# Performance work log

Measured on AMD Instinct MI355X. Metric: run time of the kernel, lower is better.

The kernel has to match this reference:

```python
import jax, jax.numpy as jnp
import numpy as np

D_MODEL = 1024
LAYER_IDX = 5
D_FF = 4096
SPARSITY = 0.9
TOKENS = 8192
IN_UP = D_MODEL * (LAYER_IDX + 1)  # 6144


def _sparse_weight(rng, out_f, in_f, sparsity):
    """Row-wise k-sparse weight matrix mimicking SparseLinear's padded-CSR:
    each output row keeps k = round(in_f*(1-sparsity)) live columns,
    values ~ U(-b, b) with b = 1/sqrt(effective_fan_in)."""
    k = max(1, round(in_f * (1.0 - sparsity)))
    bound = 1.0 / np.sqrt(max(1.0, in_f * (1.0 - sparsity)))
    scores = rng.random((out_f, in_f))
    # top-k per row -> boolean mask
    thresh = np.partition(scores, in_f - k, axis=1)[:, in_f - k][:, None]
    mask = scores >= thresh
    W = (rng.uniform(-bound, bound, (out_f, in_f)).astype(np.float32)) * mask
    return jnp.asarray(W), jnp.asarray(mask)


def setup_inputs() -> dict:
    key = jax.random.key(0)
    x = jax.random.normal(key, (TOKENS, IN_UP), dtype=jnp.float32)
    rng = np.random.default_rng(0)
    W_up, mask_up = _sparse_weight(rng, D_FF, IN_UP, SPARSITY)
    W_down, mask_down = _sparse_weight(rng, D_MODEL, D_FF, SPARSITY)
    return {"ffn_input_cat": x, "W_up": W_up, "W_down": W_down,
            "mask_up": mask_up, "mask_down": mask_down}


def reference(ffn_input_cat, W_up, W_down, mask_up, mask_down):
    # fc_down(gelu(fc_up(x))); SparseLinear == masked dense linear, no bias.
    # torch F.gelu default is the exact (erf) gelu.
    h = jax.nn.gelu(ffn_input_cat @ (W_up * mask_up).T, approximate=False)  # [T, d_ff]
    return h @ (W_down * mask_down).T  # [T, d_model]
```

## Files before the change

kernel.cpp:

```cpp
#include <hip/hip_runtime.h>
#include <cstdint>
#include <cstddef>

typedef unsigned short u16;
typedef __attribute__((ext_vector_type(8))) short  bf16x8;
typedef __attribute__((ext_vector_type(4))) float  f32x4;
typedef __attribute__((ext_vector_type(4))) unsigned short u16x4;

__device__ __forceinline__ u16 f2bf(float f) {
    unsigned u = __float_as_uint(f);
    unsigned r = (u + 0x7FFFu + ((u >> 16) & 1u)) >> 16;
    return (u16)r;
}

__device__ __forceinline__ void async_lds16(const u16* g, u16* l) {
    __builtin_amdgcn_global_load_lds(
        (const __attribute__((address_space(1))) unsigned int*)g,
        (__attribute__((address_space(3))) unsigned int*)l,
        16, 0, 0);
}

__global__ __launch_bounds__(256) void cvt3_kernel(const float* __restrict__ s0, u16* __restrict__ d0, int n0,
                                                   const float* __restrict__ s1, u16* __restrict__ d1, int n1,
                                                   const float* __restrict__ s2, u16* __restrict__ d2, int n2) {
    const int total = n0 + n1 + n2;
    for (int i = blockIdx.x * 256 + threadIdx.x; i < total; i += gridDim.x * 256) {
        const float* s; u16* d; int j = i;
        if (j < n0)            { s = s0; d = d0; }
        else if (j < n0 + n1)  { s = s1; d = d1; j -= n0; }
        else                   { s = s2; d = d2; j -= n0 + n1; }
        float4 a = ((const float4*)s)[j];
        u16x4 o;
        o[0] = f2bf(a.x); o[1] = f2bf(a.y); o[2] = f2bf(a.z); o[3] = f2bf(a.w);
        ((u16x4*)d)[j] = o;
    }
}


template<bool GELU, typename OutT, int BN>
__global__ __launch_bounds__(512, 2) void gemm_q(const u16* __restrict__ A,
                                                 const u16* __restrict__ B,
                                                 OutT* __restrict__ C,
                                                 int K, int lda, int ldb, int ldc) {
    constexpr int NI  = BN / 64;
    constexpr int NQN = NI / 2;
    __shared__ __align__(16) u16 sA[2][256 * 64];
    __shared__ __align__(16) u16 sB[2][BN * 64];

    const int tid  = threadIdx.x;
    const int wave = tid >> 6;
    const int lane = tid & 63;
    const int quad = lane >> 4;
    const int r16  = lane & 15;

    const int nwg = gridDim.x * gridDim.y;
    int lin = blockIdx.y * gridDim.x + blockIdx.x;
    lin = (lin & 7) * (nwg >> 3) + (lin >> 3);
    const int n0 = (lin % gridDim.x) * BN;
    const int m0 = (lin / gridDim.x) * 256;

    const int wm = (wave >> 2) * 128;
    const int wn = (wave & 3) * (BN / 4);

    const int srow = tid >> 3;
    const int scol = (((tid & 7) ^ (srow & 7)) << 3);
    const u16* gAs = A + (size_t)(m0 + srow) * lda + scol;
    const u16* gBs = B + (size_t)(n0 + srow) * ldb + scol;

#define STAGE_A(dst, kt) { const size_t ko_ = (size_t)(kt) * 64; \
    _Pragma("unroll") for (int i_ = 0; i_ < 4; i_++) \
        async_lds16(gAs + (size_t)(i_ * 64) * lda + ko_, (dst) + i_ * 4096 + tid * 8); }
#define STAGE_B(dst, kt) { const size_t ko_ = (size_t)(kt) * 64; \
    _Pragma("unroll") for (int i_ = 0; i_ < NI; i_++) \
        async_lds16(gBs + (size_t)(i_ * 64) * ldb + ko_, (dst) + i_ * 4096 + tid * 8); }

    const int g0 = (quad ^ (r16 & 7)) << 3;
    const int g1 = g0 ^ 32;

    struct FragT { bf16x8 a[4][2]; bf16x8 b[NQN][2]; };

#define READQ(F, Ab, Bb, qmi, qni) { \
    _Pragma("unroll") for (int i_ = 0; i_ < 4; i_++) { \
        const int ao_ = (wm + ((qmi) * 4 + i_) * 16 + r16) * 64; \
        F.a[i_][0] = *(const bf16x8*)&(Ab)[ao_ + g0]; \
        F.a[i_][1] = *(const bf16x8*)&(Ab)[ao_ + g1]; } \
    _Pragma("unroll") for (int i_ = 0; i_ < NQN; i_++) { \
        const int bo_ = (wn + ((qni) * NQN + i_) * 16 + r16) * 64; \
        F.b[i_][0] = *(const bf16x8*)&(Bb)[bo_ + g0]; \
        F.b[i_][1] = *(const bf16x8*)&(Bb)[bo_ + g1]; } }

#define LGKM0 asm volatile("s_waitcnt lgkmcnt(0)" ::: "memory"); __builtin_amdgcn_sched_barrier(0)
#define VM0   asm volatile("s_waitcnt vmcnt(0)"  ::: "memory"); __builtin_amdgcn_sched_barrier(0)
#define PIN   __builtin_amdgcn_sched_barrier(0)
#define BARR  __builtin_amdgcn_s_barrier()

#define MFMAQ(q, F) \
    __builtin_amdgcn_s_setprio(1); \
    _Pragma("unroll") for (int mi_ = 0; mi_ < 4; mi_++) \
    _Pragma("unroll") for (int ni_ = 0; ni_ < NQN; ni_++) { \
        const int am_ = ((q) & 1) * 4 + mi_; \
        const int an_ = ((q) >> 1) * NQN + ni_; \
        acc[am_][an_] = __builtin_amdgcn_mfma_f32_16x16x32_bf16( \
            F.a[mi_][0], F.b[ni_][0], acc[am_][an_], 0, 0, 0); \
        acc[am_][an_] = __builtin_amdgcn_mfma_f32_16x16x32_bf16( \
            F.a[mi_][1], F.b[ni_][1], acc[am_][an_], 0, 0, 0); } \
    __builtin_amdgcn_s_setprio(0); \
    __builtin_amdgcn_sched_barrier(0)

    f32x4 acc[8][NI] = {};
    const int NT = K / 64;

    FragT f0, f1;

    STAGE_A(&sA[0][0], 0); STAGE_B(&sB[0][0], 0);
    VM0;
    BARR; PIN;
    READQ(f0, sA[0], sB[0], 0, 0);

    for (int t = 0; t < NT; ++t) {
        const u16* Ac = sA[t & 1];
        const u16* Bc = sB[t & 1];
        u16* An = &sA[(t + 1) & 1][0];
        u16* Bn = &sB[(t + 1) & 1][0];
        const int kt = (t + 1 < NT) ? (t + 1) : 0;

        READQ(f1, Ac, Bc, 1, 0);
        STAGE_A(An, kt);
        PIN; BARR; LGKM0;
        MFMAQ(0, f0);

        READQ(f0, Ac, Bc, 0, 1);
        STAGE_B(Bn, kt);
        PIN; BARR; LGKM0;
        MFMAQ(1, f1);

        READQ(f1, Ac, Bc, 1, 1);
        PIN; BARR; LGKM0;
        MFMAQ(2, f0);

        VM0;
        BARR; PIN;
        if (t + 1 < NT) { READQ(f0, An, Bn, 0, 0); }
        PIN;
        MFMAQ(3, f1);
    }

#pragma unroll
    for (int mi = 0; mi < 8; mi++) {
#pragma unroll
        for (int r = 0; r < 4; r++) {
            size_t rowoff = (size_t)(m0 + wm + mi * 16 + quad * 4 + r) * ldc;
#pragma unroll
            for (int ni = 0; ni < NI; ni++) {
                int col = n0 + wn + ni * 16 + r16;
                float v = acc[mi][ni][r];
                if constexpr (GELU)
                    v = 0.5f * v * (1.0f + erff(v * 0.70710678118654752f));
                if constexpr (sizeof(OutT) == 2)
                    ((u16*)C)[rowoff + col] = f2bf(v);
                else
                    ((float*)C)[rowoff + col] = v;
            }
        }
    }
}

extern "C" void kernel_launch(void* const* d_in, const int* in_sizes, int n_in,
                              void* d_out, int out_size, void* d_ws, size_t ws_size,
                              hipStream_t stream) {
    const int T   = 8192;
    const int DIN = 6144;
    const int DFF = 4096;
    const int DM  = 1024;

    const float* x  = (const float*)d_in[0];
    const float* wu = (const float*)d_in[1];
    const float* wd = (const float*)d_in[2];

    u16* xb  = (u16*)d_ws;
    u16* wub = xb  + (size_t)T * DIN;
    u16* wdb = wub + (size_t)DFF * DIN;
    u16* hb  = wdb + (size_t)DM * DFF;

    const int n4x  = T * DIN / 4;
    const int n4wu = DFF * DIN / 4;
    const int n4wd = DM * DFF / 4;
    cvt3_kernel<<<8192, 256, 0, stream>>>(x, xb, n4x, wu, wub, n4wu, wd, wdb, n4wd);

    dim3 g1(DFF / 256, T / 256);
    gemm_q<true, u16, 256><<<g1, 512, 0, stream>>>(xb, wub, hb, DIN, DIN, DIN, DFF);

    dim3 g2(DM / 128, T / 256);
    gemm_q<false, float, 128><<<g2, 512, 0, stream>>>(hb, wdb, (float*)d_out,
                                                      DFF, DFF, DFF, DM);
}
```

Baseline: 953.8 us.

## Restructure GEMM main loop to prefetch two K-tiles ahead with partial vmcnt waits

Rewrites the bf16 MFMA GEMM main loop so global-to-LDS loads run two K-tiles ahead, split into per-quarter chunks issued in the middle of the MFMA phases, and waits with a partial vmcnt count instead of draining all loads. LDS read offsets are precomputed per lane, and the loop is unrolled by two with ping-pong B fragment registers. The goal is to hide global load latency better and reduce full pipeline stalls at each tile boundary. The cost is more barriers per iteration, more live registers, and stages that overwrite the current buffer, which depend on careful barrier placement for correctness.

```diff
diff --git a/kernel.cpp b/kernel.cpp
--- a/kernel.cpp
+++ b/kernel.cpp
@@ -38,14 +38,17 @@
 
 
 template<bool GELU, typename OutT, int BN>
-__global__ __launch_bounds__(512, 2) void gemm_q(const u16* __restrict__ A,
+__global__ __launch_bounds__(512, 2) void gemm_p(const u16* __restrict__ A,
                                                  const u16* __restrict__ B,
                                                  OutT* __restrict__ C,
                                                  int K, int lda, int ldb, int ldc) {
     constexpr int NI  = BN / 64;
     constexpr int NQN = NI / 2;
-    __shared__ __align__(16) u16 sA[2][256 * 64];
-    __shared__ __align__(16) u16 sB[2][BN * 64];
+    constexpr int BQ  = BN / 64;
+    constexpr int ATL = 256 * 64;
+    constexpr int BTL = BN * 64;
+    __shared__ __align__(16) u16 sAm[2 * ATL];
+    __shared__ __align__(16) u16 sBm[2 * BTL];
 
     const int tid  = threadIdx.x;
     const int wave = tid >> 6;
@@ -67,83 +70,90 @@
     const u16* gAs = A + (size_t)(m0 + srow) * lda + scol;
     const u16* gBs = B + (size_t)(n0 + srow) * ldb + scol;
 
-#define STAGE_A(dst, kt) { const size_t ko_ = (size_t)(kt) * 64; \
-    _Pragma("unroll") for (int i_ = 0; i_ < 4; i_++) \
-        async_lds16(gAs + (size_t)(i_ * 64) * lda + ko_, (dst) + i_ * 4096 + tid * 8); }
-#define STAGE_B(dst, kt) { const size_t ko_ = (size_t)(kt) * 64; \
-    _Pragma("unroll") for (int i_ = 0; i_ < NI; i_++) \
-        async_lds16(gBs + (size_t)(i_ * 64) * ldb + ko_, (dst) + i_ * 4096 + tid * 8); }
-
-    const int g0 = (quad ^ (r16 & 7)) << 3;
-    const int g1 = g0 ^ 32;
-
-    struct FragT { bf16x8 a[4][2]; bf16x8 b[NQN][2]; };
-
-#define READQ(F, Ab, Bb, qmi, qni) { \
-    _Pragma("unroll") for (int i_ = 0; i_ < 4; i_++) { \
-        const int ao_ = (wm + ((qmi) * 4 + i_) * 16 + r16) * 64; \
-        F.a[i_][0] = *(const bf16x8*)&(Ab)[ao_ + g0]; \
-        F.a[i_][1] = *(const bf16x8*)&(Ab)[ao_ + g1]; } \
-    _Pragma("unroll") for (int i_ = 0; i_ < NQN; i_++) { \
-        const int bo_ = (wn + ((qni) * NQN + i_) * 16 + r16) * 64; \
-        F.b[i_][0] = *(const bf16x8*)&(Bb)[bo_ + g0]; \
-        F.b[i_][1] = *(const bf16x8*)&(Bb)[bo_ + g1]; } }
+#define SA_U(bufbase, q, kt) async_lds16(gAs + (size_t)((q) * 64) * lda + (size_t)(kt) * 64, \
+                                         (bufbase) + (q) * 4096 + tid * 8)
+#define SB_U(bufbase, q, kt) async_lds16(gBs + (size_t)((q) * 64) * ldb + (size_t)(kt) * 64, \
+                                         (bufbase) + (q) * 4096 + tid * 8)
+
+    int oA0[4], oA1[4], oB0[NQN], oB1[NQN];
+#pragma unroll
+    for (int i = 0; i < 4; i++) {
+        int r = wm + i * 16 + r16;
+        oA0[i] = r * 64 + (((0 + quad) ^ (r & 7)) << 3);
+        oA1[i] = r * 64 + (((4 + quad) ^ (r & 7)) << 3);
+    }
+#pragma unroll
+    for (int j = 0; j < NQN; j++) {
+        int r = wn + j * 16 + r16;
+        oB0[j] = r * 64 + (((0 + quad) ^ (r & 7)) << 3);
+        oB1[j] = r * 64 + (((4 + quad) ^ (r & 7)) << 3);
+    }
+
+    f32x4 acc[8][NI] = {};
+    const int NT = K / 64;
 
 #define LGKM0 asm volatile("s_waitcnt lgkmcnt(0)" ::: "memory"); __builtin_amdgcn_sched_barrier(0)
-#define VM0   asm volatile("s_waitcnt vmcnt(0)"  ::: "memory"); __builtin_amdgcn_sched_barrier(0)
 #define PIN   __builtin_amdgcn_sched_barrier(0)
 #define BARR  __builtin_amdgcn_s_barrier()
-
-#define MFMAQ(q, F) \
+#define VMW   do { if constexpr (BN == 256) { asm volatile("s_waitcnt vmcnt(8)" ::: "memory"); } \
+                   else                     { asm volatile("s_waitcnt vmcnt(6)" ::: "memory"); } } while (0)
+
+#define RD_A(mh, Ab) { _Pragma("unroll") for (int i_ = 0; i_ < 4; i_++) { \
+        af[i_][0] = *(const bf16x8*)&(Ab)[oA0[i_] + (mh) * 4096]; \
+        af[i_][1] = *(const bf16x8*)&(Ab)[oA1[i_] + (mh) * 4096]; } }
+#define RD_B(dst, Bb, nh) { _Pragma("unroll") for (int j_ = 0; j_ < NQN; j_++) { \
+        dst[j_][0] = *(const bf16x8*)&(Bb)[oB0[j_] + (nh) * (NQN * 1024)]; \
+        dst[j_][1] = *(const bf16x8*)&(Bb)[oB1[j_] + (nh) * (NQN * 1024)]; } }
+
+#define MM(mh, nh, BF) \
     __builtin_amdgcn_s_setprio(1); \
     _Pragma("unroll") for (int mi_ = 0; mi_ < 4; mi_++) \
-    _Pragma("unroll") for (int ni_ = 0; ni_ < NQN; ni_++) { \
-        const int am_ = ((q) & 1) * 4 + mi_; \
-        const int an_ = ((q) >> 1) * NQN + ni_; \
-        acc[am_][an_] = __builtin_amdgcn_mfma_f32_16x16x32_bf16( \
-            F.a[mi_][0], F.b[ni_][0], acc[am_][an_], 0, 0, 0); \
-        acc[am_][an_] = __builtin_amdgcn_mfma_f32_16x16x32_bf16( \
-            F.a[mi_][1], F.b[ni_][1], acc[am_][an_], 0, 0, 0); } \
+    _Pragma("unroll") for (int nj_ = 0; nj_ < NQN; nj_++) { \
+        acc[(mh) * 4 + mi_][(nh) * NQN + nj_] = __builtin_amdgcn_mfma_f32_16x16x32_bf16( \
+            af[mi_][0], BF[nj_][0], acc[(mh) * 4 + mi_][(nh) * NQN + nj_], 0, 0, 0); \
+        acc[(mh) * 4 + mi_][(nh) * NQN + nj_] = __builtin_amdgcn_mfma_f32_16x16x32_bf16( \
+            af[mi_][1], BF[nj_][1], acc[(mh) * 4 + mi_][(nh) * NQN + nj_], 0, 0, 0); } \
     __builtin_amdgcn_s_setprio(0); \
     __builtin_amdgcn_sched_barrier(0)
 
-    f32x4 acc[8][NI] = {};
-    const int NT = K / 64;
-
-    FragT f0, f1;
-
-    STAGE_A(&sA[0][0], 0); STAGE_B(&sB[0][0], 0);
-    VM0;
-    BARR; PIN;
-    READQ(f0, sA[0], sB[0], 0, 0);
-
-    for (int t = 0; t < NT; ++t) {
-        const u16* Ac = sA[t & 1];
-        const u16* Bc = sB[t & 1];
-        u16* An = &sA[(t + 1) & 1][0];
-        u16* Bn = &sB[(t + 1) & 1][0];
-        const int kt = (t + 1 < NT) ? (t + 1) : 0;
-
-        READQ(f1, Ac, Bc, 1, 0);
-        STAGE_A(An, kt);
-        PIN; BARR; LGKM0;
-        MFMAQ(0, f0);
-
-        READQ(f0, Ac, Bc, 0, 1);
-        STAGE_B(Bn, kt);
-        PIN; BARR; LGKM0;
-        MFMAQ(1, f1);
-
-        READQ(f1, Ac, Bc, 1, 1);
-        PIN; BARR; LGKM0;
-        MFMAQ(2, f0);
-
-        VM0;
+    bf16x8 af[4][2], bf1[NQN][2], bf0x[NQN][2], bf0y[NQN][2];
+
+    {
+        u16* a0 = sAm; u16* b0 = sBm; u16* a1 = sAm + ATL; u16* b1 = sBm + BTL;
+#pragma unroll
+        for (int q = 0; q < 4; q++)  SA_U(a0, q, 0);
+#pragma unroll
+        for (int q = 0; q < BQ; q++) SB_U(b0, q, 0);
+#pragma unroll
+        for (int q = 0; q < 4; q++)  SA_U(a1, q, 1);
+#pragma unroll
+        for (int q = 0; q < BQ; q++) SB_U(b1, q, 1);
+        asm volatile("s_waitcnt vmcnt(0)" ::: "memory");
         BARR; PIN;
-        if (t + 1 < NT) { READQ(f0, An, Bn, 0, 0); }
-        PIN;
-        MFMAQ(3, f1);
-    }
+        RD_B(bf0x, sBm, 0);
+    }
+
+#define ITER(T_, BUF, B0C, B0N) { \
+        u16* Ab = sAm + (BUF) * ATL; \
+        u16* Bb = sBm + (BUF) * BTL; \
+        u16* Bo = sBm + ((BUF) ^ 1) * BTL; \
+        int kt2 = (T_) + 2; if (kt2 >= NT) kt2 -= NT; \
+         RD_A(0, Ab); PIN; BARR; LGKM0; MM(0, 0, B0C); PIN; BARR; \
+         RD_B(bf1, Bb, 1); SA_U(Ab, 0, kt2); SA_U(Ab, 2, kt2); \
+                 PIN; BARR; LGKM0; MM(0, 1, bf1); PIN; BARR; \
+         RD_A(1, Ab); PIN; BARR; LGKM0; MM(1, 1, bf1); PIN; BARR; \
+         SA_U(Ab, 1, kt2); SA_U(Ab, 3, kt2); \
+                 _Pragma("unroll") for (int q_ = 0; q_ < BQ; q_++) SB_U(Bb, q_, kt2); \
+                 VMW; PIN; BARR; PIN; \
+                 RD_B(B0N, Bo, 0); PIN; \
+                 MM(1, 0, B0C); PIN; BARR; \
+    }
+
+    for (int t = 0; t < NT; t += 2) {
+        ITER(t,     0, bf0x, bf0y);
+        ITER(t + 1, 1, bf0y, bf0x);
+    }
+    asm volatile("s_waitcnt vmcnt(0)" ::: "memory");
 
 #pragma unroll
     for (int mi = 0; mi < 8; mi++) {
@@ -188,9 +198,9 @@
     cvt3_kernel<<<8192, 256, 0, stream>>>(x, xb, n4x, wu, wub, n4wu, wd, wdb, n4wd);
 
     dim3 g1(DFF / 256, T / 256);
-    gemm_q<true, u16, 256><<<g1, 512, 0, stream>>>(xb, wub, hb, DIN, DIN, DIN, DFF);
+    gemm_p<true, u16, 256><<<g1, 512, 0, stream>>>(xb, wub, hb, DIN, DIN, DIN, DFF);
 
     dim3 g2(DM / 128, T / 256);
-    gemm_q<false, float, 128><<<g2, 512, 0, stream>>>(hb, wdb, (float*)d_out,
+    gemm_p<false, float, 128><<<g2, 512, 0, stream>>>(hb, wdb, (float*)d_out,
                                                       DFF, DFF, DFF, DM);
 }
```

After: 983.9 us. 1.03x slower.
